# Kernel optimization log

Measured on AMD Instinct MI355X. Metric: run time of the kernel, lower is better.

The kernel has to match this reference:

```python
import jax, jax.numpy as jnp
import numpy as np

B, S, E, H = 4, 2048, 1024, 16
D = E // H  # head dim


def setup_inputs() -> dict:
    key = jax.random.key(0)
    ks = jax.random.split(key, 6)
    sc = 1.0 / np.sqrt(E)
    return {
        "x":  jax.random.normal(ks[0], (B, S, E), dtype=jnp.float32),
        "Wk": jax.random.normal(ks[1], (E, E), dtype=jnp.float32) * sc,
        "Wq": jax.random.normal(ks[2], (E, E), dtype=jnp.float32) * sc,
        "Wv": jax.random.normal(ks[3], (E, E), dtype=jnp.float32) * sc,
        "Wo": jax.random.normal(ks[4], (E, E), dtype=jnp.float32) * sc,
        "bo": jax.random.normal(ks[5], (E,), dtype=jnp.float32) * sc,
    }


def reference(x, Wk, Wq, Wv, Wo, bo):
    b, s, e = x.shape
    # torch Linear: y = x @ W.T (weights are [out, in])
    K = x @ Wk.T
    Q = x @ Wq.T
    _V_unused = x @ Wv.T  # computed in source but discarded (V = Q.view bug)
    # split heads: [b, s, H, D] -> [b, H, s, D]
    Kh = K.reshape(b, s, H, D).transpose(0, 2, 1, 3)
    Qh = Q.reshape(b, s, H, D).transpose(0, 2, 1, 3)
    Vh = Qh  # faithful to source: V = Q.view(...)
    # scaled dot product, scaled by sqrt(embedding_size) as in source
    scores = jnp.einsum('bhqd,bhkd->bhqk', Qh, Kh) / jnp.sqrt(jnp.float32(e))
    causal = jnp.tril(jnp.ones((s, s), dtype=bool))
    scores = jnp.where(causal, scores, -jnp.inf)
    probs = jax.nn.softmax(scores, axis=-1)
    attn = jnp.einsum('bhqk,bhkd->bhqd', probs, Vh)
    attn = attn.transpose(0, 2, 1, 3).reshape(b, s, e)
    return attn @ Wo.T + bo
```

## Files before the change

kernel.cpp:

```cpp
#include <hip/hip_runtime.h>
#include <hip/hip_bf16.h>

#define PB 4
#define PS 2048
#define PE 1024
#define PH 16
#define PD 64

typedef __attribute__((ext_vector_type(8))) short bf16x8;
typedef __attribute__((ext_vector_type(4))) float f32x4;
typedef const __attribute__((address_space(1))) unsigned int* gas_t;
typedef __attribute__((address_space(3))) unsigned int* las_t;

__device__ __forceinline__ unsigned short f2bf(float f) {
  union { float f; unsigned int u; } v;
  v.f = f;
  unsigned int u = v.u;
  u += 0x7fffu + ((u >> 16) & 1u);
  return (unsigned short)(u >> 16);
}

__device__ __forceinline__ f32x4 mfma16(bf16x8 a, bf16x8 b, f32x4 c) {
  return __builtin_amdgcn_mfma_f32_16x16x32_bf16(a, b, c, 0, 0, 0);
}

#define CVT_GROUPS ((PB * PS * PE + 3 * PE * PE) / 4)
#define CVT_BLOCKS (CVT_GROUPS / 256)
__global__ __launch_bounds__(256) void cvt_kernel(
    const float* __restrict__ x, const float* __restrict__ wk,
    const float* __restrict__ wq, const float* __restrict__ wo,
    unsigned short* __restrict__ xb, unsigned short* __restrict__ wkb,
    unsigned short* __restrict__ wqb, unsigned short* __restrict__ wob) {
  const long long NX = (long long)PB * PS * PE;
  const long long NW = (long long)PE * PE;
  long long i = ((long long)blockIdx.x * 256 + threadIdx.x) * 4;
  const float* src;
  unsigned short* dst;
  long long off;
  if (i < NX)               { src = x;  dst = xb;  off = i; }
  else if (i < NX + NW)     { src = wk; dst = wkb; off = i - NX; }
  else if (i < NX + 2 * NW) { src = wq; dst = wqb; off = i - NX - NW; }
  else                      { src = wo; dst = wob; off = i - NX - 2 * NW; }
  float4 v = *(const float4*)(src + off);
  ushort4 o;
  o.x = f2bf(v.x); o.y = f2bf(v.y); o.z = f2bf(v.z); o.w = f2bf(v.w);
  *(ushort4*)(dst + off) = o;
}

__global__ __launch_bounds__(256) void gemm_qk(
    const unsigned short* __restrict__ A, const unsigned short* __restrict__ Bq,
    const unsigned short* __restrict__ Bk,
    unsigned short* __restrict__ QT, unsigned short* __restrict__ Kb) {
  const int K = PE, N = PE;
  __shared__ __attribute__((aligned(16))) unsigned short As[128 * 64];
  __shared__ __attribute__((aligned(16))) unsigned short Bqs[128 * 64];
  __shared__ __attribute__((aligned(16))) unsigned short Bks[128 * 64];
  const int tid = threadIdx.x;
  const int wave = tid >> 6, lane = tid & 63;
  const int quad = lane >> 4, ln = lane & 15;
  const int m0 = blockIdx.y * 128, n0 = blockIdx.x * 128;
  const int wm = (wave >> 1) * 64, wn = (wave & 1) * 64;

  f32x4 aq[4][4], ak[4][4];
#pragma unroll
  for (int i = 0; i < 4; ++i)
#pragma unroll
    for (int j = 0; j < 4; ++j)
#pragma unroll
      for (int r = 0; r < 4; ++r) { aq[i][j][r] = 0.f; ak[i][j][r] = 0.f; }

  for (int k0 = 0; k0 < K; k0 += 64) {
#pragma unroll
    for (int it = 0; it < 4; ++it) {
      const int idx = it * 256 + tid;
      const int row = idx >> 3, ch = idx & 7;
      const int gch = ch ^ (row & 7);
      __builtin_amdgcn_global_load_lds(
          (gas_t)(const void*)(A + (size_t)(m0 + row) * K + k0 + gch * 8),
          (las_t)(void*)((char*)As + idx * 16), 16, 0, 0);
      __builtin_amdgcn_global_load_lds(
          (gas_t)(const void*)(Bq + (size_t)(n0 + row) * K + k0 + gch * 8),
          (las_t)(void*)((char*)Bqs + idx * 16), 16, 0, 0);
      __builtin_amdgcn_global_load_lds(
          (gas_t)(const void*)(Bk + (size_t)(n0 + row) * K + k0 + gch * 8),
          (las_t)(void*)((char*)Bks + idx * 16), 16, 0, 0);
    }
    __syncthreads();
#pragma unroll
    for (int kc = 0; kc < 2; ++kc) {
      bf16x8 af[4], bqf[4], bkf[4];
#pragma unroll
      for (int t = 0; t < 4; ++t) {
        const int ra = wm + t * 16 + ln;
        const int rb = wn + t * 16 + ln;
        af[t]  = *(const bf16x8*)(As  + ra * 64 + ((kc * 4 + quad) ^ (ra & 7)) * 8);
        bqf[t] = *(const bf16x8*)(Bqs + rb * 64 + ((kc * 4 + quad) ^ (rb & 7)) * 8);
        bkf[t] = *(const bf16x8*)(Bks + rb * 64 + ((kc * 4 + quad) ^ (rb & 7)) * 8);
      }
#pragma unroll
      for (int mt = 0; mt < 4; ++mt)
#pragma unroll
        for (int nt = 0; nt < 4; ++nt) {
          aq[mt][nt] = mfma16(af[mt], bqf[nt], aq[mt][nt]);
          ak[mt][nt] = mfma16(af[mt], bkf[nt], ak[mt][nt]);
        }
    }
    __syncthreads();
  }

#pragma unroll
  for (int mt = 0; mt < 4; ++mt) {
#pragma unroll
    for (int nt = 0; nt < 4; ++nt) {
      const int row = m0 + wm + mt * 16 + quad * 4;
      const int col = n0 + wn + nt * 16 + ln;
      const int b = row >> 11, s = row & 2047;
      const int h = col >> 6, d = col & 63;
      ushort4 ov;
      ov.x = f2bf(aq[mt][nt][0]); ov.y = f2bf(aq[mt][nt][1]);
      ov.z = f2bf(aq[mt][nt][2]); ov.w = f2bf(aq[mt][nt][3]);
      *(ushort4*)(QT + (((size_t)(b * PH + h) * PD + d) * PS + s)) = ov;
#pragma unroll
      for (int r = 0; r < 4; ++r)
        Kb[(size_t)(row + r) * N + col] = f2bf(ak[mt][nt][r]);
    }
  }
}

__global__ __launch_bounds__(256) void gemm_out(
    const unsigned short* __restrict__ A, const unsigned short* __restrict__ Bm,
    const float* __restrict__ bias, float* __restrict__ Cf) {
  const int K = PE, N = PE;
  __shared__ __attribute__((aligned(16))) unsigned short As[128 * 64];
  __shared__ __attribute__((aligned(16))) unsigned short Bs[128 * 64];
  const int tid = threadIdx.x;
  const int wave = tid >> 6, lane = tid & 63;
  const int quad = lane >> 4, ln = lane & 15;
  const int m0 = blockIdx.y * 128, n0 = blockIdx.x * 128;
  const int wm = (wave >> 1) * 64, wn = (wave & 1) * 64;

  f32x4 acc[4][4];
#pragma unroll
  for (int i = 0; i < 4; ++i)
#pragma unroll
    for (int j = 0; j < 4; ++j)
#pragma unroll
      for (int r = 0; r < 4; ++r) acc[i][j][r] = 0.f;

  for (int k0 = 0; k0 < K; k0 += 64) {
#pragma unroll
    for (int it = 0; it < 4; ++it) {
      const int idx = it * 256 + tid;
      const int row = idx >> 3, ch = idx & 7;
      const int gch = ch ^ (row & 7);
      __builtin_amdgcn_global_load_lds(
          (gas_t)(const void*)(A + (size_t)(m0 + row) * K + k0 + gch * 8),
          (las_t)(void*)((char*)As + idx * 16), 16, 0, 0);
      __builtin_amdgcn_global_load_lds(
          (gas_t)(const void*)(Bm + (size_t)(n0 + row) * K + k0 + gch * 8),
          (las_t)(void*)((char*)Bs + idx * 16), 16, 0, 0);
    }
    __syncthreads();
#pragma unroll
    for (int kc = 0; kc < 2; ++kc) {
      bf16x8 af[4], bfr[4];
#pragma unroll
      for (int t = 0; t < 4; ++t) {
        const int ra = wm + t * 16 + ln;
        const int rb = wn + t * 16 + ln;
        af[t]  = *(const bf16x8*)(As + ra * 64 + ((kc * 4 + quad) ^ (ra & 7)) * 8);
        bfr[t] = *(const bf16x8*)(Bs + rb * 64 + ((kc * 4 + quad) ^ (rb & 7)) * 8);
      }
#pragma unroll
      for (int mt = 0; mt < 4; ++mt)
#pragma unroll
        for (int nt = 0; nt < 4; ++nt)
          acc[mt][nt] = mfma16(af[mt], bfr[nt], acc[mt][nt]);
    }
    __syncthreads();
  }

#pragma unroll
  for (int mt = 0; mt < 4; ++mt) {
#pragma unroll
    for (int nt = 0; nt < 4; ++nt) {
      const int row = m0 + wm + mt * 16 + quad * 4;
      const int col = n0 + wn + nt * 16 + ln;
      const float bv = bias[col];
#pragma unroll
      for (int r = 0; r < 4; ++r)
        Cf[(size_t)(row + r) * N + col] = acc[mt][nt][r] + bv;
    }
  }
}

__global__ __launch_bounds__(256) void attn_kernel(
    const unsigned short* __restrict__ QT,
    const unsigned short* __restrict__ Kb,
    unsigned short* __restrict__ Ab) {
  __shared__ __attribute__((aligned(16))) unsigned short Ks[64 * 64];
  __shared__ __attribute__((aligned(16))) unsigned short Vs[64 * 64];
  __shared__ __attribute__((aligned(16))) unsigned short Ps[4][32 * 72];

  const int tid = threadIdx.x;
  const int wave = tid >> 6, lane = tid & 63;
  const int quad = lane >> 4, ln = lane & 15;
  const int h = blockIdx.y, b = blockIdx.z;
  const size_t hoff  = ((size_t)b * PS) * PE + (size_t)h * PD;
  const size_t hofft = ((size_t)(b * PH + h) * PD) * PS;
  const float CEXP = 0.045084220f;
  const int srow = tid >> 3, sch = tid & 7;

  for (int pass = 0; pass < 2; ++pass) {
    const int qt = pass ? (int)blockIdx.x : 15 - (int)blockIdx.x;
    const int qw0 = qt * 128 + wave * 32;

    bf16x8 qfr[2][2];
#pragma unroll
    for (int nq = 0; nq < 2; ++nq)
#pragma unroll
      for (int c = 0; c < 2; ++c) {
        union { unsigned short u[8]; bf16x8 v; } tmp;
#pragma unroll
        for (int j = 0; j < 8; ++j)
          tmp.u[j] = QT[hofft + (size_t)(c * 32 + quad * 8 + j) * PS +
                        qw0 + nq * 16 + ln];
        qfr[nq][c] = tmp.v;
      }

    f32x4 o[2][4];
    float psum[2];
#pragma unroll
    for (int mq = 0; mq < 2; ++mq)
#pragma unroll
      for (int td = 0; td < 4; ++td)
#pragma unroll
        for (int r = 0; r < 4; ++r) o[mq][td][r] = 0.f;
    psum[0] = psum[1] = 0.f;

    const int ktend = 2 * qt + 2;
    for (int kt = 0; kt < ktend; ++kt) {
      const int k0 = kt * 64;

#pragma unroll
      for (int r = 0; r < 2; ++r) {
        const int row = r * 32 + srow;
        const int gch = sch ^ (row & 7);
        __builtin_amdgcn_global_load_lds(
            (gas_t)(const void*)(Kb + hoff + (size_t)(k0 + row) * PE + gch * 8),
            (las_t)(void*)((char*)Ks + (r * 256 + tid) * 16), 16, 0, 0);
        __builtin_amdgcn_global_load_lds(
            (gas_t)(const void*)(QT + hofft + (size_t)row * PS + k0 + gch * 8),
            (las_t)(void*)((char*)Vs + (r * 256 + tid) * 16), 16, 0, 0);
      }
      __syncthreads();

      f32x4 sacc[4][2];
#pragma unroll
      for (int mk = 0; mk < 4; ++mk)
#pragma unroll
        for (int nq = 0; nq < 2; ++nq)
#pragma unroll
          for (int r = 0; r < 4; ++r) sacc[mk][nq][r] = 0.f;
#pragma unroll
      for (int c = 0; c < 2; ++c) {
        const int ch = ((c * 4 + quad) ^ (ln & 7)) * 8;
        bf16x8 kf[4];
#pragma unroll
        for (int mk = 0; mk < 4; ++mk)
          kf[mk] = *(const bf16x8*)(Ks + (mk * 16 + ln) * 64 + ch);
#pragma unroll
        for (int mk = 0; mk < 4; ++mk)
#pragma unroll
          for (int nq = 0; nq < 2; ++nq)
            sacc[mk][nq] = mfma16(kf[mk], qfr[nq][c], sacc[mk][nq]);
      }

      const bool edge = (k0 + 63) > qw0;
#pragma unroll
      for (int mk = 0; mk < 4; ++mk)
#pragma unroll
        for (int nq = 0; nq < 2; ++nq) {
          float p[4];
#pragma unroll
          for (int r = 0; r < 4; ++r)
            p[r] = __builtin_amdgcn_exp2f(sacc[mk][nq][r] * CEXP);
          if (edge) {
            const int qg = qw0 + nq * 16 + ln;
#pragma unroll
            for (int r = 0; r < 4; ++r) {
              const int kg = k0 + mk * 16 + quad * 4 + r;
              p[r] = (kg <= qg) ? p[r] : 0.f;
            }
          }
          psum[nq] += (p[0] + p[1]) + (p[2] + p[3]);
          union { __hip_bfloat162 h2; unsigned int u; } u01, u23;
          u01.h2 = __float22bfloat162_rn(float2{p[0], p[1]});
          u23.h2 = __float22bfloat162_rn(float2{p[2], p[3]});
          *(uint2*)(&Ps[wave][(nq * 16 + ln) * 72 + mk * 16 + quad * 4]) =
              uint2{u01.u, u23.u};
        }

#pragma unroll
      for (int c = 0; c < 2; ++c) {
        const int ch = ((c * 4 + quad) ^ (ln & 7)) * 8;
        bf16x8 pf0 = *(const bf16x8*)(&Ps[wave][ln * 72 + c * 32 + quad * 8]);
        bf16x8 pf1 = *(const bf16x8*)(&Ps[wave][(16 + ln) * 72 + c * 32 + quad * 8]);
#pragma unroll
        for (int td = 0; td < 4; ++td) {
          bf16x8 vfd = *(const bf16x8*)(Vs + (td * 16 + ln) * 64 + ch);
          o[0][td] = mfma16(pf0, vfd, o[0][td]);
          o[1][td] = mfma16(pf1, vfd, o[1][td]);
        }
      }
      __syncthreads();
    }

#pragma unroll
    for (int nq = 0; nq < 2; ++nq) {
      psum[nq] += __shfl_xor(psum[nq], 16, 64);
      psum[nq] += __shfl_xor(psum[nq], 32, 64);
    }
    float invq[2][4];
#pragma unroll
    for (int mq = 0; mq < 2; ++mq)
#pragma unroll
      for (int r = 0; r < 4; ++r)
        invq[mq][r] = 1.f / __shfl(psum[mq], quad * 4 + r, 64);

#pragma unroll
    for (int mq = 0; mq < 2; ++mq)
#pragma unroll
      for (int r = 0; r < 4; ++r) {
        const int qg = qw0 + mq * 16 + quad * 4 + r;
#pragma unroll
        for (int td = 0; td < 4; ++td)
          Ab[hoff + (size_t)qg * PE + td * 16 + ln] =
              f2bf(o[mq][td][r] * invq[mq][r]);
      }
  }
}

extern "C" void kernel_launch(void* const* d_in, const int* in_sizes, int n_in,
                              void* d_out, int out_size, void* d_ws, size_t ws_size,
                              hipStream_t stream) {
  (void)in_sizes; (void)n_in; (void)out_size; (void)ws_size;
  const float* x  = (const float*)d_in[0];
  const float* Wk = (const float*)d_in[1];
  const float* Wq = (const float*)d_in[2];
  const float* Wo = (const float*)d_in[4];
  const float* bo = (const float*)d_in[5];
  float* out = (float*)d_out;

  char* ws = (char*)d_ws;
  unsigned short* xb  = (unsigned short*)(ws);
  unsigned short* wkb = (unsigned short*)(ws + (16u << 20));
  unsigned short* wqb = (unsigned short*)(ws + (18u << 20));
  unsigned short* wob = (unsigned short*)(ws + (20u << 20));
  unsigned short* QT  = (unsigned short*)(ws + (22u << 20));
  unsigned short* Kb  = (unsigned short*)(ws + (38u << 20));
  unsigned short* Ab  = xb;

  const int M = PB * PS;

  cvt_kernel<<<dim3(CVT_BLOCKS), dim3(256), 0, stream>>>(
      x, Wk, Wq, Wo, xb, wkb, wqb, wob);

  gemm_qk<<<dim3(PE / 128, M / 128), dim3(256), 0, stream>>>(
      xb, wqb, wkb, QT, Kb);

  attn_kernel<<<dim3(8, PH, PB), dim3(256), 0, stream>>>(QT, Kb, Ab);

  gemm_out<<<dim3(PE / 128, M / 128), dim3(256), 0, stream>>>(
      Ab, wob, bo, out);
}
```

Before: 261.2 us.

## Shrink attention query tile to 64 rows and fold softmax scale into K

Each attention block now handles 64 query rows, 16 per wave, instead of 128. This doubles the grid to 16x16x4 blocks, and the paired-pass scheme now spans 32 query chunks. The softmax exponent scale is multiplied into K when the QK GEMM writes it, which removes a multiply per score in the inner loop. The smaller tile improves parallelism and causal load balance and cuts register use. In exchange, each K/V tile staged into LDS now serves half as many queries, so global/LDS traffic per FLOP doubles. Pre-scaling K before the bf16 rounding changes the precision slightly.

```diff
diff --git a/kernel.cpp b/kernel.cpp
--- a/kernel.cpp
+++ b/kernel.cpp
@@ -108,6 +108,7 @@
     __syncthreads();
   }
 
+  const float CEXP = 0.045084220f;
 #pragma unroll
   for (int mt = 0; mt < 4; ++mt) {
 #pragma unroll
@@ -122,7 +123,7 @@
       *(ushort4*)(QT + (((size_t)(b * PH + h) * PD + d) * PS + s)) = ov;
 #pragma unroll
       for (int r = 0; r < 4; ++r)
-        Kb[(size_t)(row + r) * N + col] = f2bf(ak[mt][nt][r]);
+        Kb[(size_t)(row + r) * N + col] = f2bf(ak[mt][nt][r] * CEXP);
     }
   }
 }
@@ -200,7 +201,7 @@
     unsigned short* __restrict__ Ab) {
   __shared__ __attribute__((aligned(16))) unsigned short Ks[64 * 64];
   __shared__ __attribute__((aligned(16))) unsigned short Vs[64 * 64];
-  __shared__ __attribute__((aligned(16))) unsigned short Ps[4][32 * 72];
+  __shared__ __attribute__((aligned(16))) unsigned short Ps[4][16 * 72];
 
   const int tid = threadIdx.x;
   const int wave = tid >> 6, lane = tid & 63;
@@ -208,37 +209,30 @@
   const int h = blockIdx.y, b = blockIdx.z;
   const size_t hoff  = ((size_t)b * PS) * PE + (size_t)h * PD;
   const size_t hofft = ((size_t)(b * PH + h) * PD) * PS;
-  const float CEXP = 0.045084220f;
   const int srow = tid >> 3, sch = tid & 7;
 
   for (int pass = 0; pass < 2; ++pass) {
-    const int qt = pass ? (int)blockIdx.x : 15 - (int)blockIdx.x;
-    const int qw0 = qt * 128 + wave * 32;
-
-    bf16x8 qfr[2][2];
-#pragma unroll
-    for (int nq = 0; nq < 2; ++nq)
-#pragma unroll
-      for (int c = 0; c < 2; ++c) {
-        union { unsigned short u[8]; bf16x8 v; } tmp;
-#pragma unroll
-        for (int j = 0; j < 8; ++j)
-          tmp.u[j] = QT[hofft + (size_t)(c * 32 + quad * 8 + j) * PS +
-                        qw0 + nq * 16 + ln];
-        qfr[nq][c] = tmp.v;
-      }
-
-    f32x4 o[2][4];
-    float psum[2];
-#pragma unroll
-    for (int mq = 0; mq < 2; ++mq)
-#pragma unroll
-      for (int td = 0; td < 4; ++td)
-#pragma unroll
-        for (int r = 0; r < 4; ++r) o[mq][td][r] = 0.f;
-    psum[0] = psum[1] = 0.f;
-
-    const int ktend = 2 * qt + 2;
+    const int qc = pass ? (int)blockIdx.x : 31 - (int)blockIdx.x;
+    const int qw0 = qc * 64 + wave * 16;
+
+    bf16x8 qfr[2];
+#pragma unroll
+    for (int c = 0; c < 2; ++c) {
+      union { unsigned short u[8]; bf16x8 v; } tmp;
+#pragma unroll
+      for (int j = 0; j < 8; ++j)
+        tmp.u[j] = QT[hofft + (size_t)(c * 32 + quad * 8 + j) * PS + qw0 + ln];
+      qfr[c] = tmp.v;
+    }
+
+    f32x4 o[4];
+    float psum = 0.f;
+#pragma unroll
+    for (int td = 0; td < 4; ++td)
+#pragma unroll
+      for (int r = 0; r < 4; ++r) o[td][r] = 0.f;
+
+    const int ktend = qc + 1;
     for (int kt = 0; kt < ktend; ++kt) {
       const int k0 = kt * 64;
 
@@ -255,13 +249,11 @@
       }
       __syncthreads();
 
-      f32x4 sacc[4][2];
+      f32x4 sacc[4];
 #pragma unroll
       for (int mk = 0; mk < 4; ++mk)
 #pragma unroll
-        for (int nq = 0; nq < 2; ++nq)
-#pragma unroll
-          for (int r = 0; r < 4; ++r) sacc[mk][nq][r] = 0.f;
+        for (int r = 0; r < 4; ++r) sacc[mk][r] = 0.f;
 #pragma unroll
       for (int c = 0; c < 2; ++c) {
         const int ch = ((c * 4 + quad) ^ (ln & 7)) * 8;
@@ -271,73 +263,60 @@
           kf[mk] = *(const bf16x8*)(Ks + (mk * 16 + ln) * 64 + ch);
 #pragma unroll
         for (int mk = 0; mk < 4; ++mk)
-#pragma unroll
-          for (int nq = 0; nq < 2; ++nq)
-            sacc[mk][nq] = mfma16(kf[mk], qfr[nq][c], sacc[mk][nq]);
+          sacc[mk] = mfma16(kf[mk], qfr[c], sacc[mk]);
       }
 
       const bool edge = (k0 + 63) > qw0;
 #pragma unroll
-      for (int mk = 0; mk < 4; ++mk)
-#pragma unroll
-        for (int nq = 0; nq < 2; ++nq) {
-          float p[4];
-#pragma unroll
-          for (int r = 0; r < 4; ++r)
-            p[r] = __builtin_amdgcn_exp2f(sacc[mk][nq][r] * CEXP);
-          if (edge) {
-            const int qg = qw0 + nq * 16 + ln;
-#pragma unroll
-            for (int r = 0; r < 4; ++r) {
-              const int kg = k0 + mk * 16 + quad * 4 + r;
-              p[r] = (kg <= qg) ? p[r] : 0.f;
-            }
+      for (int mk = 0; mk < 4; ++mk) {
+        float p[4];
+#pragma unroll
+        for (int r = 0; r < 4; ++r)
+          p[r] = __builtin_amdgcn_exp2f(sacc[mk][r]);
+        if (edge) {
+          const int qg = qw0 + ln;
+#pragma unroll
+          for (int r = 0; r < 4; ++r) {
+            const int kg = k0 + mk * 16 + quad * 4 + r;
+            p[r] = (kg <= qg) ? p[r] : 0.f;
           }
-          psum[nq] += (p[0] + p[1]) + (p[2] + p[3]);
-          union { __hip_bfloat162 h2; unsigned int u; } u01, u23;
-          u01.h2 = __float22bfloat162_rn(float2{p[0], p[1]});
-          u23.h2 = __float22bfloat162_rn(float2{p[2], p[3]});
-          *(uint2*)(&Ps[wave][(nq * 16 + ln) * 72 + mk * 16 + quad * 4]) =
-              uint2{u01.u, u23.u};
         }
+        psum += (p[0] + p[1]) + (p[2] + p[3]);
+        union { __hip_bfloat162 h2; unsigned int u; } u01, u23;
+        u01.h2 = __float22bfloat162_rn(float2{p[0], p[1]});
+        u23.h2 = __float22bfloat162_rn(float2{p[2], p[3]});
+        *(uint2*)(&Ps[wave][ln * 72 + mk * 16 + quad * 4]) =
+            uint2{u01.u, u23.u};
+      }
 
 #pragma unroll
       for (int c = 0; c < 2; ++c) {
         const int ch = ((c * 4 + quad) ^ (ln & 7)) * 8;
-        bf16x8 pf0 = *(const bf16x8*)(&Ps[wave][ln * 72 + c * 32 + quad * 8]);
-        bf16x8 pf1 = *(const bf16x8*)(&Ps[wave][(16 + ln) * 72 + c * 32 + quad * 8]);
+        bf16x8 pf = *(const bf16x8*)(&Ps[wave][ln * 72 + c * 32 + quad * 8]);
 #pragma unroll
         for (int td = 0; td < 4; ++td) {
           bf16x8 vfd = *(const bf16x8*)(Vs + (td * 16 + ln) * 64 + ch);
-          o[0][td] = mfma16(pf0, vfd, o[0][td]);
-          o[1][td] = mfma16(pf1, vfd, o[1][td]);
+          o[td] = mfma16(pf, vfd, o[td]);
         }
       }
       __syncthreads();
     }
 
-#pragma unroll
-    for (int nq = 0; nq < 2; ++nq) {
-      psum[nq] += __shfl_xor(psum[nq], 16, 64);
-      psum[nq] += __shfl_xor(psum[nq], 32, 64);
-    }
-    float invq[2][4];
-#pragma unroll
-    for (int mq = 0; mq < 2; ++mq)
-#pragma unroll
-      for (int r = 0; r < 4; ++r)
-        invq[mq][r] = 1.f / __shfl(psum[mq], quad * 4 + r, 64);
-
-#pragma unroll
-    for (int mq = 0; mq < 2; ++mq)
-#pragma unroll
-      for (int r = 0; r < 4; ++r) {
-        const int qg = qw0 + mq * 16 + quad * 4 + r;
-#pragma unroll
-        for (int td = 0; td < 4; ++td)
-          Ab[hoff + (size_t)qg * PE + td * 16 + ln] =
-              f2bf(o[mq][td][r] * invq[mq][r]);
-      }
+    psum += __shfl_xor(psum, 16, 64);
+    psum += __shfl_xor(psum, 32, 64);
+    float invq[4];
+#pragma unroll
+    for (int r = 0; r < 4; ++r)
+      invq[r] = 1.f / __shfl(psum, quad * 4 + r, 64);
+
+#pragma unroll
+    for (int r = 0; r < 4; ++r) {
+      const int qg = qw0 + quad * 4 + r;
+#pragma unroll
+      for (int td = 0; td < 4; ++td)
+        Ab[hoff + (size_t)qg * PE + td * 16 + ln] =
+            f2bf(o[td][r] * invq[r]);
+    }
   }
 }
 
@@ -369,7 +348,7 @@
   gemm_qk<<<dim3(PE / 128, M / 128), dim3(256), 0, stream>>>(
       xb, wqb, wkb, QT, Kb);
 
-  attn_kernel<<<dim3(8, PH, PB), dim3(256), 0, stream>>>(QT, Kb, Ab);
+  attn_kernel<<<dim3(16, PH, PB), dim3(256), 0, stream>>>(QT, Kb, Ab);
 
   gemm_out<<<dim3(PE / 128, M / 128), dim3(256), 0, stream>>>(
       Ab, wob, bo, out);
```

Measured after the change: 257.9 us. About the same (-1.2%).
